# Kernel tuning notes

Hardware: AMD Instinct MI355X
Metric: run time of the kernel (lower is better)

The kernel has to match this reference:

```python
import jax, jax.numpy as jnp
import numpy as np

KEY_SIZE = 512


def setup_inputs() -> dict:
    key = jax.random.key(0)
    ks = jax.random.split(key, 4)
    B, T, C = 8, 2048, 512
    s = 0.02
    return {
        "x": jax.random.normal(ks[0], (B, T, C), dtype=jnp.float32),
        "Wq": jax.random.normal(ks[1], (KEY_SIZE, C), dtype=jnp.float32) * s,
        "bq": jnp.zeros((KEY_SIZE,), dtype=jnp.float32),
        "Wk": jax.random.normal(ks[2], (KEY_SIZE, C), dtype=jnp.float32) * s,
        "bk": jnp.zeros((KEY_SIZE,), dtype=jnp.float32),
        "Wv": jax.random.normal(ks[3], (KEY_SIZE, C), dtype=jnp.float32) * s,
        "bv": jnp.zeros((KEY_SIZE,), dtype=jnp.float32),
    }


def reference(x, Wq, bq, Wk, bk, Wv, bv):
    # x: [B, T, C]; Linear(y) = y @ W.T + b (torch convention)
    q = jnp.einsum("btc,kc->btk", x, Wq) + bq  # [B, T, K]
    k = jnp.einsum("btc,kc->btk", x, Wk) + bk  # [B, T, K]
    v = jnp.einsum("btc,vc->btv", x, Wv) + bv  # [B, T, V]

    scores = jnp.einsum("bqk,bsk->bqs", q, k)  # [B, Tq, Tk]
    T = x.shape[1]
    # mask[j, i] = 1 if i > j  -> strict upper triangle masked with -inf
    mask = jnp.triu(jnp.ones((T, T), dtype=bool), k=1)
    scores = jnp.where(mask[None, :, :], -jnp.inf, scores)
    # NOTE: original divides by sqrt(key_size) AFTER masking, and takes
    # softmax over dim=1 (the QUERY axis) — faithfully reproduced.
    probs = jax.nn.softmax(scores / jnp.sqrt(jnp.asarray(KEY_SIZE, scores.dtype)), axis=1)
    attn = jnp.einsum("bqs,bsv->bqv", probs, v)  # [B, T, V]
    return jnp.concatenate([x, attn], axis=2)  # [B, T, C + V]
```

## Files before the change

### kernel.cpp

```cpp
#include <hip/hip_runtime.h>

#define BATCH 8
#define TSEQ  2048
#define CDIM  512
#define MTOK  (BATCH*TSEQ)
#define NTRI  136

typedef __attribute__((ext_vector_type(8))) short bf16x8;
typedef __attribute__((ext_vector_type(4))) float f32x4;

__device__ __forceinline__ unsigned short f2bf(float f) {
    union { float f; unsigned int u; } v; v.f = f;
    unsigned int r = v.u + 0x7FFF + ((v.u >> 16) & 1);
    return (unsigned short)(r >> 16);
}
__device__ __forceinline__ float bfl(unsigned short u) {
    union { unsigned int i; float f; } v; v.i = ((unsigned int)u) << 16; return v.f;
}

__device__ __forceinline__ f32x4 fzero() { f32x4 z = {0.f, 0.f, 0.f, 0.f}; return z; }

__device__ __forceinline__ void gl2lds16(const void* g, void* l) {
    __builtin_amdgcn_global_load_lds(
        (const __attribute__((address_space(1))) unsigned int*)g,
        (__attribute__((address_space(3))) unsigned int*)l, 16, 0, 0);
}

__device__ __forceinline__ void stage_tile(const unsigned short* src, size_t ld,
                                           unsigned short* buf, int t) {
    const unsigned short* s0 = src + (size_t)(t >> 2) * ld + (t & 3) * 8;
    gl2lds16(s0, &buf[t * 8]);
    gl2lds16(s0 + (size_t)64 * ld, &buf[2048 + t * 8]);
}

#define LGKM0() do { asm volatile("s_waitcnt lgkmcnt(0)" ::: "memory"); \
                     __builtin_amdgcn_sched_barrier(0); } while (0)
#define VMCNT(n) do { asm volatile("s_waitcnt vmcnt(" #n ")" ::: "memory"); \
                      __builtin_amdgcn_sched_barrier(0); } while (0)
#define BARRIER() do { __builtin_amdgcn_sched_barrier(0); \
                       __builtin_amdgcn_s_barrier(); \
                       __builtin_amdgcn_sched_barrier(0); } while (0)

__global__ __launch_bounds__(256) void k_convert_x(const float* __restrict__ x,
                                                   unsigned short* __restrict__ xb,
                                                   float* __restrict__ out) {
    int i = blockIdx.x * blockDim.x + threadIdx.x;
    float4 v = ((const float4*)x)[i];
    ushort4 o;
    o.x = f2bf(v.x); o.y = f2bf(v.y); o.z = f2bf(v.z); o.w = f2bf(v.w);
    ((ushort4*)xb)[i] = o;
    int e = i * 4;
    int row = e >> 9;
    int c   = e & 511;
    *(float4*)(out + (size_t)row * 1024 + c) = v;
}

__global__ __launch_bounds__(256) void k_convert_w3(const float* __restrict__ Wq,
                                                    const float* __restrict__ Wk,
                                                    const float* __restrict__ Wv,
                                                    unsigned short* __restrict__ wb) {
    int i = blockIdx.x * 256 + threadIdx.x;
    int m = i >> 16;
    const float* w = (m == 0) ? Wq : ((m == 1) ? Wk : Wv);
    float4 v = ((const float4*)w)[i & 65535];
    ushort4 o;
    o.x = f2bf(v.x); o.y = f2bf(v.y); o.z = f2bf(v.z); o.w = f2bf(v.w);
    ((ushort4*)wb)[i] = o;
}

__global__ __launch_bounds__(512, 2) void k_qkv(const unsigned short* __restrict__ xb,
                                                const unsigned short* __restrict__ Wcat,
                                                const float* __restrict__ bq,
                                                const float* __restrict__ bk,
                                                const float* __restrict__ bv,
                                                unsigned short* __restrict__ QKb,
                                                unsigned short* __restrict__ Vt) {
    __shared__ __align__(16) unsigned short lds[65536];
    int orig = blockIdx.x;
    int flat = (orig & 7) * 48 + (orig >> 3);
    int mt = flat / 6, nt = flat - mt * 6;
    int m0 = mt * 256, n0 = nt * 256;
    int t = threadIdx.x, w = t >> 6, lane = t & 63;
    int quad = lane >> 4, lane16 = lane & 15;
    int wr = w >> 2, wc = w & 3;
    int l3 = lane >> 3;
    int sl = (lane & 7) ^ l3;
    int rswz = (lane16 & 7) << 3;

    const unsigned short* Abase = xb + (size_t)m0 * 512;
    const unsigned short* Bbase = Wcat + (size_t)n0 * 512;

    f32x4 acc[8][4];
#pragma unroll
    for (int i = 0; i < 8; i++)
#pragma unroll
        for (int j = 0; j < 4; j++) acc[i][j] = fzero();

    auto stage_half = [&](const unsigned short* panel, int r0, int kt,
                          unsigned short* buf) {
#pragma unroll
        for (int i = 0; i < 2; ++i) {
            int q = i * 8 + w;
            gl2lds16(panel + (size_t)(r0 + q * 8 + l3) * 512 + kt * 64 + sl * 8,
                     &buf[q * 512 + lane * 8]);
        }
    };
    auto ldsA = [&](int c, int h) { return &lds[c * 32768 + h * 8192]; };
    auto ldsB = [&](int c, int h) { return &lds[c * 32768 + 16384 + h * 8192]; };

    stage_half(Bbase, 0,   0, ldsB(0, 0));
    stage_half(Bbase, 128, 0, ldsB(0, 1));
    stage_half(Abase, 0,   0, ldsA(0, 0));
    stage_half(Abase, 128, 0, ldsA(0, 1));
    __builtin_amdgcn_sched_barrier(0);
    stage_half(Bbase, 0,   1, ldsB(1, 0));
    stage_half(Bbase, 128, 1, ldsB(1, 1));
    stage_half(Abase, 0,   1, ldsA(1, 0));
    VMCNT(6);
    BARRIER();

    bf16x8 afr[4][2];
    bf16x8 bfr[2][2][2];

    auto ldA = [&](int c, int mh) {
        const unsigned short* As = &lds[c * 32768];
        int rowb = wr * 128 + mh * 64 + lane16;
#pragma unroll
        for (int mi = 0; mi < 4; ++mi)
#pragma unroll
            for (int ks = 0; ks < 2; ++ks)
                afr[mi][ks] = *(const bf16x8*)&As[(rowb + mi * 16) * 64 +
                                                  ((ks * 32 + quad * 8) ^ rswz)];
    };
    auto ldB = [&](int c) {
        const unsigned short* Bs = &lds[c * 32768 + 16384];
        int rowb = wc * 64 + lane16;
#pragma unroll
        for (int ni = 0; ni < 4; ++ni)
#pragma unroll
            for (int ks = 0; ks < 2; ++ks)
                bfr[ni >> 1][ni & 1][ks] = *(const bf16x8*)&Bs[(rowb + ni * 16) * 64 +
                                                  ((ks * 32 + quad * 8) ^ rswz)];
    };
    auto quadmma = [&](int mh, int nh) {
        __builtin_amdgcn_s_setprio(1);
#pragma unroll
        for (int mi = 0; mi < 4; ++mi)
#pragma unroll
            for (int nin = 0; nin < 2; ++nin)
#pragma unroll
                for (int ks = 0; ks < 2; ++ks)
                    acc[mh * 4 + mi][nh * 2 + nin] = __builtin_amdgcn_mfma_f32_16x16x32_bf16(
                        afr[mi][ks], bfr[nh][nin][ks], acc[mh * 4 + mi][nh * 2 + nin], 0, 0, 0);
        __builtin_amdgcn_s_setprio(0);
    };

#pragma unroll
    for (int i = 0; i < 4; ++i) {
        const int tE = 2 * i + 2;
        const int tO = 2 * i + 3;
        ldA(0, 0); ldB(0);
        stage_half(Abase, 128, 2 * i + 1, ldsA(1, 1));
        BARRIER(); LGKM0();
        quadmma(0, 0);
        BARRIER();
        if (tE < 8) stage_half(Bbase, 0, tE, ldsB(0, 0));
        BARRIER();
        quadmma(0, 1);
        BARRIER();
        ldA(0, 1);
        if (tE < 8) stage_half(Bbase, 128, tE, ldsB(0, 1));
        BARRIER(); LGKM0();
        quadmma(1, 0);
        BARRIER();
        if (tE < 8) stage_half(Abase, 0, tE, ldsA(0, 0));
        if (i < 3) { VMCNT(6); } else { VMCNT(0); }
        BARRIER();
        quadmma(1, 1);
        BARRIER();
        ldA(1, 0); ldB(1);
        if (tE < 8) stage_half(Abase, 128, tE, ldsA(0, 1));
        BARRIER(); LGKM0();
        quadmma(0, 0);
        BARRIER();
        if (tO < 8) stage_half(Bbase, 0, tO, ldsB(1, 0));
        BARRIER();
        quadmma(0, 1);
        BARRIER();
        ldA(1, 1);
        if (tO < 8) stage_half(Bbase, 128, tO, ldsB(1, 1));
        BARRIER(); LGKM0();
        quadmma(1, 0);
        BARRIER();
        if (tO < 8) stage_half(Abase, 0, tO, ldsA(1, 0));
        if (i < 3) { VMCNT(6); }
        BARRIER();
        quadmma(1, 1);
        BARRIER();
    }
    __syncthreads();

    int which = n0 >> 9;
    if (which < 2) {
        const float* bias = which ? bk : bq;
        unsigned short* T = &lds[w * 4608];
        int colBase = which * 512 + (n0 & 511) + wc * 64;
#pragma unroll
        for (int p = 0; p < 2; ++p) {
#pragma unroll
            for (int ni = 0; ni < 4; ++ni) {
                float bb = bias[(n0 & 511) + wc * 64 + ni * 16 + lane16];
#pragma unroll
                for (int mi2 = 0; mi2 < 4; ++mi2)
#pragma unroll
                    for (int r = 0; r < 4; ++r)
                        T[(mi2 * 16 + quad * 4 + r) * 72 + ni * 16 + lane16] =
                            f2bf(acc[p * 4 + mi2][ni][r] + bb);
            }
#pragma unroll
            for (int i = 0; i < 8; ++i) {
                int rl = i * 8 + l3;
                int cl = (lane & 7) * 8;
                int m = m0 + wr * 128 + p * 64 + rl;
                *(uint4*)(QKb + (size_t)m * 1024 + colBase + cl) = *(const uint4*)&T[rl * 72 + cl];
            }
        }
    } else {
        unsigned short* T = &lds[w * 4352];
        int b = m0 >> 11, tbase = (m0 & 2047) + wr * 128;
        int nv = (n0 & 511) + wc * 64;
#pragma unroll
        for (int p = 0; p < 2; ++p) {
#pragma unroll
            for (int j = 0; j < 2; ++j) {
                int ni = p * 2 + j;
                float bb = bv[nv + ni * 16 + lane16];
                int vl = j * 16 + lane16;
#pragma unroll
                for (int mi = 0; mi < 8; ++mi)
#pragma unroll
                    for (int r = 0; r < 4; ++r)
                        T[vl * 136 + mi * 16 + quad * 4 + r] = f2bf(acc[mi][ni][r] + bb);
            }
#pragma unroll
            for (int i = 0; i < 8; ++i) {
                int vl = i * 4 + quad;
                int tl = lane16 * 8;
                int v = nv + p * 32 + vl;
                *(uint4*)(Vt + ((size_t)(b * 512 + v)) * 2048 + tbase + tl) =
                    *(const uint4*)&T[vl * 136 + tl];
            }
            __syncthreads();
        }
    }
}

__global__ __launch_bounds__(256) void k_score(const unsigned short* __restrict__ QKb,
                                               unsigned short* __restrict__ Pbuf,
                                               float* __restrict__ colsum) {
    __shared__ __align__(16) unsigned short lds[16384];
    int orig = blockIdx.x;
    int bb  = orig & 7;
    int idx = orig >> 3;
    int qt = (int)((sqrtf(8.0f * idx + 1.0f) - 1.0f) * 0.5f);
    while ((qt + 1) * (qt + 2) / 2 <= idx) qt++;
    while (qt * (qt + 1) / 2 > idx) qt--;
    int st = idx - qt * (qt + 1) / 2;
    int q0 = qt * 128, s0 = st * 128;

    int t = threadIdx.x, w = t >> 6, lane = t & 63, quad = lane >> 4, lane16 = lane & 15;
    int rowHalf = (w >> 1) * 64, colHalf = (w & 1) * 64;
    const unsigned short* Qrows = QKb + ((size_t)(bb * 2048 + q0)) * 1024;
    const unsigned short* Krows = QKb + ((size_t)(bb * 2048 + s0)) * 1024 + 512;

    f32x4 acc[4][4];
#pragma unroll
    for (int i = 0; i < 4; i++)
#pragma unroll
        for (int j = 0; j < 4; j++) acc[i][j] = fzero();

    stage_tile(Qrows, 1024, lds, t);
    stage_tile(Krows, 1024, lds + 4096, t);
    __syncthreads();
    int cur = 0;
    for (int k0 = 0; k0 < CDIM; k0 += 32) {
        unsigned short* As = lds + cur * 8192;
        unsigned short* Bs = As + 4096;
        if (k0 + 32 < CDIM) {
            unsigned short* An = lds + (cur ^ 1) * 8192;
            stage_tile(Qrows + k0 + 32, 1024, An, t);
            stage_tile(Krows + k0 + 32, 1024, An + 4096, t);
        }
        bf16x8 a[4], b[4];
#pragma unroll
        for (int mi = 0; mi < 4; mi++)
            a[mi] = *(const bf16x8*)&As[(rowHalf + mi * 16 + lane16) * 32 + quad * 8];
#pragma unroll
        for (int ni = 0; ni < 4; ni++)
            b[ni] = *(const bf16x8*)&Bs[(colHalf + ni * 16 + lane16) * 32 + quad * 8];
#pragma unroll
        for (int mi = 0; mi < 4; mi++)
#pragma unroll
            for (int ni = 0; ni < 4; ni++)
                acc[mi][ni] = __builtin_amdgcn_mfma_f32_16x16x32_bf16(a[mi], b[ni], acc[mi][ni], 0, 0, 0);
        __syncthreads();
        cur ^= 1;
    }

    const float scale = 0.044194173824159216f;
    unsigned short* T = &lds[w * 4096];
    float csum[4] = {0.f, 0.f, 0.f, 0.f};
#pragma unroll
    for (int ni = 0; ni < 4; ni++) {
        int s = s0 + colHalf + ni * 16 + lane16;
#pragma unroll
        for (int mi = 0; mi < 4; mi++)
#pragma unroll
            for (int r = 0; r < 4; r++) {
                int q = q0 + rowHalf + mi * 16 + quad * 4 + r;
                float p = 0.0f;
                if (s <= q) { p = __expf(acc[mi][ni][r] * scale); csum[ni] += p; }
                T[(mi * 16 + quad * 4 + r) * 64 + ni * 16 + lane16] = f2bf(p);
            }
    }
#pragma unroll
    for (int ni = 0; ni < 4; ni++) {
        float v = csum[ni];
        v += __shfl_xor(v, 16);
        v += __shfl_xor(v, 32);
        if (quad == 0)
            unsafeAtomicAdd(&colsum[bb * 2048 + s0 + colHalf + ni * 16 + lane16], v);
    }
    __syncthreads();
    unsigned short* tile = Pbuf + ((size_t)(bb * NTRI + idx)) * 16384;
#pragma unroll
    for (int i = 0; i < 8; i++) {
        int rl = i * 8 + (lane >> 3);
        int cl = (lane & 7) * 8;
        *(uint4*)(tile + (rowHalf + rl) * 128 + colHalf + cl) = *(const uint4*)&T[rl * 64 + cl];
    }
}

__global__ __launch_bounds__(256) void k_invcs(float* __restrict__ cs) {
    int i = blockIdx.x * 256 + threadIdx.x;
    cs[i] = 1.0f / cs[i];
}

__global__ __launch_bounds__(256) void k_vscale(unsigned short* __restrict__ Vt,
                                                const float* __restrict__ inv) {
    int idx = blockIdx.x * 256 + threadIdx.x;
    int s8  = idx & 255;
    int row = idx >> 8;
    int b   = row >> 9;
    uint4 raw = ((const uint4*)Vt)[idx];
    const float* ip = inv + b * TSEQ + s8 * 8;
    unsigned int rr[4] = {raw.x, raw.y, raw.z, raw.w};
    unsigned int oo[4];
#pragma unroll
    for (int j = 0; j < 4; j++) {
        float f0 = bfl((unsigned short)(rr[j] & 0xffff)) * ip[j * 2];
        float f1 = bfl((unsigned short)(rr[j] >> 16))    * ip[j * 2 + 1];
        oo[j] = (unsigned int)f2bf(f0) | ((unsigned int)f2bf(f1) << 16);
    }
    uint4 o = {oo[0], oo[1], oo[2], oo[3]};
    ((uint4*)Vt)[idx] = o;
}

__global__ __launch_bounds__(256) void k_attn(const unsigned short* __restrict__ Pbuf,
                                              const unsigned short* __restrict__ Vt,
                                              float* __restrict__ out) {
    __shared__ __align__(16) unsigned short lds[16384];
    int i = blockIdx.x;
    int slot = i & 255, half = i >> 8;
    int qt = half ? (15 - (slot >> 5)) : (slot >> 5);
    int bv = slot & 31;
    int bb = bv >> 2;
    int v0 = (bv & 3) * 128;
    int t = threadIdx.x, w = t >> 6, lane = t & 63, quad = lane >> 4, lane16 = lane & 15;
    int rowHalf = (w >> 1) * 64, colHalf = (w & 1) * 64;

    const unsigned short* Pb = Pbuf + ((size_t)(bb * NTRI + qt * (qt + 1) / 2)) * 16384;
    const unsigned short* Vb = Vt + ((size_t)(bb * 512 + v0)) * 2048;

    f32x4 acc[4][4];
#pragma unroll
    for (int ii = 0; ii < 4; ii++)
#pragma unroll
        for (int j = 0; j < 4; j++) acc[ii][j] = fzero();

    int Kend = (qt + 1) * 128;
    stage_tile(Pb, 128, lds, t);
    stage_tile(Vb, 2048, lds + 4096, t);
    __syncthreads();
    int cur = 0;
    for (int k0 = 0; k0 < Kend; k0 += 32) {
        unsigned short* As = lds + cur * 8192;
        unsigned short* Bs = As + 4096;
        int k1 = k0 + 32;
        if (k1 < Kend) {
            unsigned short* An = lds + (cur ^ 1) * 8192;
            stage_tile(Pb + (size_t)(k1 >> 7) * 16384 + (k1 & 127), 128, An, t);
            stage_tile(Vb + k1, 2048, An + 4096, t);
        }
        bf16x8 a[4], b[4];
#pragma unroll
        for (int mi = 0; mi < 4; mi++)
            a[mi] = *(const bf16x8*)&As[(rowHalf + mi * 16 + lane16) * 32 + quad * 8];
#pragma unroll
        for (int ni = 0; ni < 4; ni++)
            b[ni] = *(const bf16x8*)&Bs[(colHalf + ni * 16 + lane16) * 32 + quad * 8];
#pragma unroll
        for (int mi = 0; mi < 4; mi++)
#pragma unroll
            for (int ni = 0; ni < 4; ni++)
                acc[mi][ni] = __builtin_amdgcn_mfma_f32_16x16x32_bf16(a[mi], b[ni], acc[mi][ni], 0, 0, 0);
        __syncthreads();
        cur ^= 1;
    }

#pragma unroll
    for (int mi = 0; mi < 4; mi++)
#pragma unroll
        for (int ni = 0; ni < 4; ni++)
#pragma unroll
            for (int r = 0; r < 4; r++) {
                int q = qt * 128 + rowHalf + mi * 16 + quad * 4 + r;
                int v = v0 + colHalf + ni * 16 + lane16;
                out[((size_t)(bb * 2048 + q)) * 1024 + 512 + v] = acc[mi][ni][r];
            }
}

extern "C" void kernel_launch(void* const* d_in, const int* in_sizes, int n_in,
                              void* d_out, int out_size, void* d_ws, size_t ws_size,
                              hipStream_t stream) {
    const float* x  = (const float*)d_in[0];
    const float* Wq = (const float*)d_in[1];
    const float* bq = (const float*)d_in[2];
    const float* Wk = (const float*)d_in[3];
    const float* bk = (const float*)d_in[4];
    const float* Wv = (const float*)d_in[5];
    const float* bv = (const float*)d_in[6];
    float* out = (float*)d_out;

    char* ws = (char*)d_ws;
    size_t off = 0;
    auto alloc = [&](size_t bytes) -> void* {
        void* p = ws + off;
        off += (bytes + 255) & ~(size_t)255;
        return p;
    };
    unsigned short* QKb = (unsigned short*)alloc((size_t)MTOK * 1024 * 2);
    unsigned short* Vt  = (unsigned short*)alloc((size_t)MTOK * CDIM * 2);
    float* colsum = (float*)alloc((size_t)BATCH * TSEQ * 4);
    size_t mark = off;
    unsigned short* Wcat = (unsigned short*)alloc((size_t)3 * CDIM * CDIM * 2);
    unsigned short* xb   = (unsigned short*)alloc((size_t)MTOK * CDIM * 2);
    unsigned short* Pbuf = (unsigned short*)(ws + mark);
    (void)ws_size;

    k_convert_x<<<(MTOK * CDIM / 4) / 256, 256, 0, stream>>>(x, xb, out);
    k_convert_w3<<<(3 * CDIM * CDIM / 4) / 256, 256, 0, stream>>>(Wq, Wk, Wv, Wcat);

    k_qkv<<<384, 512, 0, stream>>>(xb, Wcat, bq, bk, bv, QKb, Vt);

    hipMemsetAsync(colsum, 0, (size_t)BATCH * TSEQ * 4, stream);
    k_score<<<1088, 256, 0, stream>>>(QKb, Pbuf, colsum);

    k_invcs<<<(BATCH * TSEQ) / 256, 256, 0, stream>>>(colsum);
    k_vscale<<<(MTOK * CDIM / 8) / 256, 256, 0, stream>>>(Vt, colsum);

    k_attn<<<512, 256, 0, stream>>>(Pbuf, Vt, out);
}
```

Baseline: 216.3 us.

## Use 64-wide K tiles with XOR-swizzled LDS in score and attention GEMMs

The score and attention GEMM kernels now stage 64-element K slices instead of 32, using an XOR swizzle on the 16-byte chunk index in LDS, with matching swizzled reads. This halves the number of barriers and loop iterations per tile and is meant to avoid LDS bank conflicts, at the cost of doubling LDS per block (64 KB), which may reduce occupancy. The attention kernel also reorders its block-to-(qt, batch/v) mapping so neighbouring blocks share batch and value columns across different query tiles.

```diff
diff --git a/kernel.cpp b/kernel.cpp
--- a/kernel.cpp
+++ b/kernel.cpp
@@ -26,11 +26,15 @@
         (__attribute__((address_space(3))) unsigned int*)l, 16, 0, 0);
 }
 
-__device__ __forceinline__ void stage_tile(const unsigned short* src, size_t ld,
-                                           unsigned short* buf, int t) {
-    const unsigned short* s0 = src + (size_t)(t >> 2) * ld + (t & 3) * 8;
-    gl2lds16(s0, &buf[t * 8]);
-    gl2lds16(s0 + (size_t)64 * ld, &buf[2048 + t * 8]);
+__device__ __forceinline__ void stage_sw64(const unsigned short* src, size_t ld,
+                                           unsigned short* buf, int w, int lane) {
+    int l3 = lane >> 3;
+    int sl = (lane & 7) ^ l3;
+#pragma unroll
+    for (int i = 0; i < 4; ++i) {
+        int q = i * 4 + w;
+        gl2lds16(src + (size_t)(q * 8 + l3) * ld + sl * 8, &buf[q * 512 + lane * 8]);
+    }
 }
 
 #define LGKM0() do { asm volatile("s_waitcnt lgkmcnt(0)" ::: "memory"); \
@@ -258,7 +262,7 @@
 __global__ __launch_bounds__(256) void k_score(const unsigned short* __restrict__ QKb,
                                                unsigned short* __restrict__ Pbuf,
                                                float* __restrict__ colsum) {
-    __shared__ __align__(16) unsigned short lds[16384];
+    __shared__ __align__(16) unsigned short lds[32768];
     int orig = blockIdx.x;
     int bb  = orig & 7;
     int idx = orig >> 3;
@@ -270,6 +274,7 @@
 
     int t = threadIdx.x, w = t >> 6, lane = t & 63, quad = lane >> 4, lane16 = lane & 15;
     int rowHalf = (w >> 1) * 64, colHalf = (w & 1) * 64;
+    int rswz = (lane16 & 7) << 3;
     const unsigned short* Qrows = QKb + ((size_t)(bb * 2048 + q0)) * 1024;
     const unsigned short* Krows = QKb + ((size_t)(bb * 2048 + s0)) * 1024 + 512;
 
@@ -279,32 +284,39 @@
 #pragma unroll
         for (int j = 0; j < 4; j++) acc[i][j] = fzero();
 
-    stage_tile(Qrows, 1024, lds, t);
-    stage_tile(Krows, 1024, lds + 4096, t);
+    stage_sw64(Qrows, 1024, &lds[0], w, lane);
+    stage_sw64(Krows, 1024, &lds[8192], w, lane);
     __syncthreads();
-    int cur = 0;
-    for (int k0 = 0; k0 < CDIM; k0 += 32) {
-        unsigned short* As = lds + cur * 8192;
-        unsigned short* Bs = As + 4096;
-        if (k0 + 32 < CDIM) {
-            unsigned short* An = lds + (cur ^ 1) * 8192;
-            stage_tile(Qrows + k0 + 32, 1024, An, t);
-            stage_tile(Krows + k0 + 32, 1024, An + 4096, t);
+    for (int k0 = 0; k0 < CDIM; k0 += 64) {
+        int c = (k0 >> 6) & 1;
+        const unsigned short* As = &lds[c * 16384];
+        const unsigned short* Bs = As + 8192;
+        if (k0 + 64 < CDIM) {
+            stage_sw64(Qrows + k0 + 64, 1024, &lds[(c ^ 1) * 16384], w, lane);
+            stage_sw64(Krows + k0 + 64, 1024, &lds[(c ^ 1) * 16384 + 8192], w, lane);
         }
-        bf16x8 a[4], b[4];
+        bf16x8 a[4][2], b[4][2];
 #pragma unroll
         for (int mi = 0; mi < 4; mi++)
-            a[mi] = *(const bf16x8*)&As[(rowHalf + mi * 16 + lane16) * 32 + quad * 8];
+#pragma unroll
+            for (int ks = 0; ks < 2; ks++)
+                a[mi][ks] = *(const bf16x8*)&As[(rowHalf + mi * 16 + lane16) * 64 +
+                                                ((ks * 32 + quad * 8) ^ rswz)];
 #pragma unroll
         for (int ni = 0; ni < 4; ni++)
-            b[ni] = *(const bf16x8*)&Bs[(colHalf + ni * 16 + lane16) * 32 + quad * 8];
+#pragma unroll
+            for (int ks = 0; ks < 2; ks++)
+                b[ni][ks] = *(const bf16x8*)&Bs[(colHalf + ni * 16 + lane16) * 64 +
+                                                ((ks * 32 + quad * 8) ^ rswz)];
 #pragma unroll
         for (int mi = 0; mi < 4; mi++)
 #pragma unroll
             for (int ni = 0; ni < 4; ni++)
-                acc[mi][ni] = __builtin_amdgcn_mfma_f32_16x16x32_bf16(a[mi], b[ni], acc[mi][ni], 0, 0, 0);
+#pragma unroll
+                for (int ks = 0; ks < 2; ks++)
+                    acc[mi][ni] = __builtin_amdgcn_mfma_f32_16x16x32_bf16(
+                        a[mi][ks], b[ni][ks], acc[mi][ni], 0, 0, 0);
         __syncthreads();
-        cur ^= 1;
     }
 
     const float scale = 0.044194173824159216f;
@@ -369,15 +381,16 @@
 __global__ __launch_bounds__(256) void k_attn(const unsigned short* __restrict__ Pbuf,
                                               const unsigned short* __restrict__ Vt,
                                               float* __restrict__ out) {
-    __shared__ __align__(16) unsigned short lds[16384];
+    __shared__ __align__(16) unsigned short lds[32768];
     int i = blockIdx.x;
     int slot = i & 255, half = i >> 8;
-    int qt = half ? (15 - (slot >> 5)) : (slot >> 5);
-    int bv = slot & 31;
+    int qt = half ? (15 - (slot & 7)) : (slot & 7);
+    int bv = slot >> 3;
     int bb = bv >> 2;
     int v0 = (bv & 3) * 128;
     int t = threadIdx.x, w = t >> 6, lane = t & 63, quad = lane >> 4, lane16 = lane & 15;
     int rowHalf = (w >> 1) * 64, colHalf = (w & 1) * 64;
+    int rswz = (lane16 & 7) << 3;
 
     const unsigned short* Pb = Pbuf + ((size_t)(bb * NTRI + qt * (qt + 1) / 2)) * 16384;
     const unsigned short* Vb = Vt + ((size_t)(bb * 512 + v0)) * 2048;
@@ -389,33 +402,41 @@
         for (int j = 0; j < 4; j++) acc[ii][j] = fzero();
 
     int Kend = (qt + 1) * 128;
-    stage_tile(Pb, 128, lds, t);
-    stage_tile(Vb, 2048, lds + 4096, t);
+    stage_sw64(Pb, 128, &lds[0], w, lane);
+    stage_sw64(Vb, 2048, &lds[8192], w, lane);
     __syncthreads();
-    int cur = 0;
-    for (int k0 = 0; k0 < Kend; k0 += 32) {
-        unsigned short* As = lds + cur * 8192;
-        unsigned short* Bs = As + 4096;
-        int k1 = k0 + 32;
+    for (int k0 = 0; k0 < Kend; k0 += 64) {
+        int c = (k0 >> 6) & 1;
+        const unsigned short* As = &lds[c * 16384];
+        const unsigned short* Bs = As + 8192;
+        int k1 = k0 + 64;
         if (k1 < Kend) {
-            unsigned short* An = lds + (cur ^ 1) * 8192;
-            stage_tile(Pb + (size_t)(k1 >> 7) * 16384 + (k1 & 127), 128, An, t);
-            stage_tile(Vb + k1, 2048, An + 4096, t);
+            stage_sw64(Pb + (size_t)(k1 >> 7) * 16384 + (k1 & 127), 128,
+                       &lds[(c ^ 1) * 16384], w, lane);
+            stage_sw64(Vb + k1, 2048, &lds[(c ^ 1) * 16384 + 8192], w, lane);
         }
-        bf16x8 a[4], b[4];
+        bf16x8 a[4][2], b[4][2];
 #pragma unroll
         for (int mi = 0; mi < 4; mi++)
-            a[mi] = *(const bf16x8*)&As[(rowHalf + mi * 16 + lane16) * 32 + quad * 8];
+#pragma unroll
+            for (int ks = 0; ks < 2; ks++)
+                a[mi][ks] = *(const bf16x8*)&As[(rowHalf + mi * 16 + lane16) * 64 +
+                                                ((ks * 32 + quad * 8) ^ rswz)];
 #pragma unroll
         for (int ni = 0; ni < 4; ni++)
-            b[ni] = *(const bf16x8*)&Bs[(colHalf + ni * 16 + lane16) * 32 + quad * 8];
+#pragma unroll
+            for (int ks = 0; ks < 2; ks++)
+                b[ni][ks] = *(const bf16x8*)&Bs[(colHalf + ni * 16 + lane16) * 64 +
+                                                ((ks * 32 + quad * 8) ^ rswz)];
 #pragma unroll
         for (int mi = 0; mi < 4; mi++)
 #pragma unroll
             for (int ni = 0; ni < 4; ni++)
-                acc[mi][ni] = __builtin_amdgcn_mfma_f32_16x16x32_bf16(a[mi], b[ni], acc[mi][ni], 0, 0, 0);
+#pragma unroll
+                for (int ks = 0; ks < 2; ks++)
+                    acc[mi][ni] = __builtin_amdgcn_mfma_f32_16x16x32_bf16(
+                        a[mi][ks], b[ni][ks], acc[mi][ni], 0, 0, 0);
         __syncthreads();
-        cur ^= 1;
     }
 
 #pragma unroll
```

Result: no change. 214.6 us (-0.8%).
